# Optimization experiments

Measured on AMD Instinct MI355X. Metric: run time of the kernel, lower is better.

Reference implementation:

```python
import jax, jax.numpy as jnp
import numpy as np

# dims
B, S, V, H, D, I, L, SL, P = 1, 2048, 32000, 1024, 512, 4096, 2, 32, 4096
DECAY_FAST, DECAY_SLOW, CONS_RATE, CONS_EVERY = 0.9, 0.99, 0.1, 10


def _ln(x, g, b):
    m = x.mean(-1, keepdims=True)
    v = ((x - m) ** 2).mean(-1, keepdims=True)
    return (x - m) * jax.lax.rsqrt(v + 1e-5) * g + b


def _memory_scan(items, gates, fast0, slow0):
    # items [B,S,D], gates [B,S,SL]; sequential per-timestep memory update
    cons = (jnp.arange(items.shape[1]) % CONS_EVERY) == 0
    def step(carry, x):
        fast, slow = carry
        item, gate, c = x
        fast = DECAY_FAST * fast + gate[:, :, None] * item[:, None, :]
        slow = jnp.where(c, DECAY_SLOW * slow + CONS_RATE * fast, slow)
        fast = jnp.where(c, (1.0 - CONS_RATE) * fast, fast)
        return (fast, slow), None
    (fast, slow), _ = jax.lax.scan(
        step, (fast0, slow0),
        (items.transpose(1, 0, 2), gates.transpose(1, 0, 2), cons))
    return fast, slow


def _forward(input_ids, fast_states, slow_states, emb, pos_emb, W_item, b_item,
             W_q, b_q, rh_W1, rh_b1, rh_W2, rh_b2, gate_W, gate_b, W_out, b_out,
             ln1_g, ln1_b, ffn_W1, ffn_b1, ffn_W2, ffn_b2, ln2_g, ln2_b, fln_g, fln_b):
    b, s = input_ids.shape
    h = emb[input_ids] + pos_emb[:s][None]  # [B,S,H]
    new_fast, new_slow = [], []
    for l in range(W_item.shape[0]):
        items = h @ W_item[l] + b_item[l]          # [B,S,D]
        query = h @ W_q[l] + b_q[l]                # [B,S,H]
        # retrieval head -> unit-norm unbinding keys
        k1 = jax.nn.gelu(items @ rh_W1[l] + rh_b1[l])
        keys = k1 @ rh_W2[l] + rh_b2[l]
        keys = keys / (jnp.linalg.norm(keys, axis=-1, keepdims=True) + 1e-6)
        fast0, slow0 = fast_states[l], slow_states[l]  # [B,SL,D]
        # retrieval uses the initial (constant-within-sequence) states, so it
        # vectorizes over seq: slot attention + hadamard unbinding
        mem = jnp.concatenate([fast0, slow0], axis=1)  # [B,2*SL,D]
        scores = jnp.einsum('bsd,bnd->bsn', keys, mem) / jnp.sqrt(jnp.float32(D))
        attn = jax.nn.softmax(scores, axis=-1)
        retrieved = jnp.einsum('bsn,bnd->bsd', attn, mem) * keys  # [B,S,D]
        gates = jax.nn.sigmoid(jnp.concatenate([h, retrieved], -1) @ gate_W[l] + gate_b[l])
        fast_gates = gates[..., :SL]
        fast, slow = _memory_scan(items, fast_gates, fast0, slow0)
        new_fast.append(fast)
        new_slow.append(slow)
        out = jnp.concatenate([query, retrieved], -1) @ W_out[l] + b_out[l]
        h = _ln(h + out, ln1_g[l], ln1_b[l])
        ffn = jax.nn.gelu(h @ ffn_W1[l] + ffn_b1[l]) @ ffn_W2[l] + ffn_b2[l]
        h = _ln(h + ffn, ln2_g[l], ln2_b[l])
    h = _ln(h, fln_g, fln_b)
    logits = jnp.einsum('bsh,vh->bsv', h, emb)  # tied lm_head
    return logits, jnp.stack(new_fast), jnp.stack(new_slow)


def setup_inputs() -> dict:
    key = jax.random.key(0)
    def rn(i, shape, scale=0.02):
        return jax.random.normal(jax.random.fold_in(key, i), shape, dtype=jnp.float32) * scale
    z = lambda shape: jnp.zeros(shape, jnp.float32)
    return dict(
        input_ids=jax.random.randint(jax.random.fold_in(key, 0), (B, S), 0, V),
        fast_states=rn(100, (L, B, SL, D), 0.5),
        slow_states=rn(101, (L, B, SL, D), 0.5),
        emb=rn(1, (V, H)),
        pos_emb=rn(2, (P, H)),
        W_item=rn(3, (L, H, D)), b_item=z((L, D)),
        W_q=rn(4, (L, H, H)), b_q=z((L, H)),
        rh_W1=rn(5, (L, D, 2 * D)), rh_b1=z((L, 2 * D)),
        rh_W2=rn(6, (L, 2 * D, D)), rh_b2=z((L, D)),
        gate_W=rn(7, (L, H + D, 2 * SL)), gate_b=z((L, 2 * SL)),
        W_out=rn(8, (L, H + D, H)), b_out=z((L, H)),
        ln1_g=jnp.ones((L, H)), ln1_b=z((L, H)),
        ffn_W1=rn(9, (L, H, I)), ffn_b1=z((L, I)),
        ffn_W2=rn(10, (L, I, H)), ffn_b2=z((L, H)),
        ln2_g=jnp.ones((L, H)), ln2_b=z((L, H)),
        fln_g=jnp.ones((H,)), fln_b=z((H,)),
    )


def reference(input_ids, fast_states, slow_states, emb, pos_emb, W_item, b_item,
              W_q, b_q, rh_W1, rh_b1, rh_W2, rh_b2, gate_W, gate_b, W_out, b_out,
              ln1_g, ln1_b, ffn_W1, ffn_b1, ffn_W2, ffn_b2, ln2_g, ln2_b, fln_g, fln_b):
    return _forward(input_ids, fast_states, slow_states, emb, pos_emb, W_item, b_item,
                    W_q, b_q, rh_W1, rh_b1, rh_W2, rh_b2, gate_W, gate_b, W_out, b_out,
                    ln1_g, ln1_b, ffn_W1, ffn_b1, ffn_W2, ffn_b2, ln2_g, ln2_b, fln_g, fln_b)
```

## Files before the change

kernel.cpp:

```cpp
#include <hip/hip_runtime.h>
#include <hip/hip_bf16.h>
#include <stdint.h>

typedef __hip_bfloat16 bf16;
typedef float f32x4 __attribute__((ext_vector_type(4)));
typedef short s16x8 __attribute__((ext_vector_type(8)));
typedef short s16x4 __attribute__((ext_vector_type(4)));

#define DEV __device__ __forceinline__

static constexpr int S_ = 2048, H_ = 1024, D_ = 512, I_ = 4096, V_ = 32000;
static constexpr int SLn = 32, Lc = 2;
static constexpr size_t LOGITS_N = (size_t)S_ * V_;

DEV float gelu_f(float x) {
    float x3 = x * x * x;
    return 0.5f * x * (1.f + tanhf(0.7978845608028654f * (x + 0.044715f * x3)));
}

#define AS1(p) ((const __attribute__((address_space(1))) void*)(uintptr_t)(p))
#define AS3(p) ((__attribute__((address_space(3))) void*)(uint32_t)(uintptr_t)(p))

template <int BM, int BN, int TH, int WM, int WN, int FLAGS>
__global__ __launch_bounds__(TH, (TH == 512) ? 2 : 3) void gemm_p4(
    const bf16* __restrict__ A, int lda, const bf16* __restrict__ BT,
    const float* __restrict__ bias, float* __restrict__ Cf, int ldf,
    bf16* __restrict__ Cb, int ldb2, int K, int Mt, int Nt) {
    constexpr int FM = BM / (WM * 16), FN = BN / (WN * 16);
    constexpr int CA = (BM * 4) / TH, CB = (BN * 4) / TH, CH = CA + CB;
    constexpr int BUFS = (BM + BN) * 32;
    __shared__ short lds[4 * BUFS];
    const int tid = threadIdx.x, lane = tid & 63;
    const int wm = (tid >> 6) / WN, wn = (tid >> 6) % WN;

    int nwg = Mt * Nt;
    int bid = blockIdx.x, wgid = bid;
    if ((nwg & 7) == 0) {
        int cpx = nwg >> 3;
        wgid = (bid & 7) * cpx + (bid >> 3);
    }
    const int m0 = (wgid % Mt) * BM, n0 = (wgid / Mt) * BN;

    const bf16* aS[CA];
    const bf16* bS[CB];
#pragma unroll
    for (int c = 0; c < CA; ++c) {
        int L = (c * TH + tid) * 16;
        int sidx = L >> 10, w = L & 1023;
        int r16 = w >> 6;
        int c2 = (w & 63) ^ (((r16 >> 3) & 1) << 5);
        aS[c] = A + (size_t)(m0 + sidx * 16 + r16) * lda + (c2 >> 1);
    }
#pragma unroll
    for (int c = 0; c < CB; ++c) {
        int L = (c * TH + tid) * 16;
        int sidx = L >> 10, w = L & 1023;
        int r16 = w >> 6;
        int c2 = (w & 63) ^ (((r16 >> 3) & 1) << 5);
        bS[c] = BT + (size_t)(n0 + sidx * 16 + r16) * K + (c2 >> 1);
    }

    auto stage = [&](int kt) {
        short* dst = &lds[(kt & 3) * BUFS];
#pragma unroll
        for (int c = 0; c < CA; ++c)
            __builtin_amdgcn_global_load_lds(AS1(aS[c] + kt * 32), AS3(dst + (c * TH + tid) * 8), 16, 0, 0);
        short* dstB = dst + BM * 32;
#pragma unroll
        for (int c = 0; c < CB; ++c)
            __builtin_amdgcn_global_load_lds(AS1(bS[c] + kt * 32), AS3(dstB + (c * TH + tid) * 8), 16, 0, 0);
    };

    const int laneoff = ((lane & 15) * 64 + ((((lane >> 4) * 8) ^ (((lane >> 3) & 1) << 4)) << 1)) >> 1;

    f32x4 acc[FM][FN];
#pragma unroll
    for (int i = 0; i < FM; i++)
#pragma unroll
        for (int j = 0; j < FN; j++)
#pragma unroll
            for (int r = 0; r < 4; r++) acc[i][j][r] = 0.f;

    const int NT = K >> 5;
    stage(0);
    stage(1);
    stage(2);
    for (int t = 0; t < NT; ++t) {
        if (t + 3 < NT) stage(t + 3);
        const int rem = NT - 1 - t;
        if (rem >= 3)
            asm volatile("s_waitcnt vmcnt(%0)" ::"n"(3 * CH) : "memory");
        else if (rem == 2)
            asm volatile("s_waitcnt vmcnt(%0)" ::"n"(2 * CH) : "memory");
        else if (rem == 1)
            asm volatile("s_waitcnt vmcnt(%0)" ::"n"(CH) : "memory");
        else
            asm volatile("s_waitcnt vmcnt(0)" ::: "memory");
        __builtin_amdgcn_s_barrier();

        const short* as = &lds[(t & 3) * BUFS];
        const short* bs = as + BM * 32;
        s16x8 af[FM], bf[FN];
#pragma unroll
        for (int i = 0; i < FM; i++) af[i] = *(const s16x8*)&as[(wm * FM + i) * 512 + laneoff];
#pragma unroll
        for (int j = 0; j < FN; j++) bf[j] = *(const s16x8*)&bs[(wn * FN + j) * 512 + laneoff];
        __builtin_amdgcn_s_setprio(1);
#pragma unroll
        for (int i = 0; i < FM; i++)
#pragma unroll
            for (int j = 0; j < FN; j++)
                acc[i][j] = __builtin_amdgcn_mfma_f32_16x16x32_bf16(af[i], bf[j], acc[i][j], 0, 0, 0);
        __builtin_amdgcn_s_setprio(0);
        __builtin_amdgcn_s_barrier();
    }

#pragma unroll
    for (int i = 0; i < FM; i++) {
        int gr0 = m0 + (wm * FM + i) * 16 + ((lane >> 4) << 2);
#pragma unroll
        for (int j = 0; j < FN; j++) {
            int gc = n0 + (wn * FN + j) * 16 + (lane & 15);
            float bv = (FLAGS & 1) ? bias[gc] : 0.f;
#pragma unroll
            for (int r = 0; r < 4; r++) {
                float v = acc[i][j][r] + bv;
                if (FLAGS & 2) v = gelu_f(v);
                if (FLAGS & 4) Cf[(size_t)(gr0 + r) * ldf + gc] = v;
                if (FLAGS & 8) Cb[(size_t)(gr0 + r) * ldb2 + gc] = __float2bfloat16(v);
            }
        }
    }
}

__global__ __launch_bounds__(256) void transpose_bf16_kernel(const float* __restrict__ W,
                                                             bf16* __restrict__ WT, int K, int N) {
    __shared__ float t[32][33];
    int tx = threadIdx.x & 31, ty = threadIdx.x >> 5;
    int kb = blockIdx.y * 32, nb = blockIdx.x * 32;
#pragma unroll
    for (int i = 0; i < 4; i++)
        t[ty + 8 * i][tx] = W[(size_t)(kb + ty + 8 * i) * N + nb + tx];
    __syncthreads();
#pragma unroll
    for (int i = 0; i < 4; i++)
        WT[(size_t)(nb + ty + 8 * i) * K + kb + tx] = __float2bfloat16(t[tx][ty + 8 * i]);
}

__global__ void conv_bf16_kernel(const float* __restrict__ src, bf16* __restrict__ dst) {
    size_t i = (size_t)blockIdx.x * 256 + threadIdx.x;
    f32x4 v = ((const f32x4*)src)[i];
    s16x4 o;
#pragma unroll
    for (int j = 0; j < 4; j++) {
        bf16 h = __float2bfloat16(v[j]);
        o[j] = *(short*)&h;
    }
    ((s16x4*)dst)[i] = o;
}

__global__ void embed_kernel(const int* __restrict__ ids, const float* __restrict__ emb,
                             const float* __restrict__ pos, float* __restrict__ hF,
                             bf16* __restrict__ hB) {
    int t = blockIdx.x, tid = threadIdx.x;
    int id = ids[t];
    f32x4 v = ((const f32x4*)(emb + (size_t)id * H_))[tid];
    f32x4 q = ((const f32x4*)(pos + (size_t)t * H_))[tid];
    v = v + q;
    ((f32x4*)(hF + (size_t)t * H_))[tid] = v;
    s16x4 o;
#pragma unroll
    for (int j = 0; j < 4; j++) {
        bf16 h = __float2bfloat16(v[j]);
        o[j] = *(short*)&h;
    }
    ((s16x4*)(hB + (size_t)t * 1536))[tid] = o;
}

__global__ __launch_bounds__(256) void ln_kernel(const float* __restrict__ x,
                                                 const float* __restrict__ res,
                                                 const float* __restrict__ g,
                                                 const float* __restrict__ b,
                                                 float* __restrict__ of, bf16* __restrict__ ob,
                                                 int ldo) {
    __shared__ float red[8];
    int row = blockIdx.x, tid = threadIdx.x, lane = tid & 63, wid = tid >> 6;
    const float* xr = x + (size_t)row * H_;
    float v[4];
#pragma unroll
    for (int j = 0; j < 4; j++) {
        int c = tid + 256 * j;
        v[j] = xr[c] + (res ? res[(size_t)row * H_ + c] : 0.f);
    }
    float s = v[0] + v[1] + v[2] + v[3];
#pragma unroll
    for (int o = 32; o; o >>= 1) s += __shfl_xor(s, o);
    if (!lane) red[wid] = s;
    __syncthreads();
    float mean = (red[0] + red[1] + red[2] + red[3]) * (1.f / H_);
    float q = 0.f;
#pragma unroll
    for (int j = 0; j < 4; j++) {
        float d = v[j] - mean;
        q += d * d;
    }
#pragma unroll
    for (int o = 32; o; o >>= 1) q += __shfl_xor(q, o);
    if (!lane) red[4 + wid] = q;
    __syncthreads();
    float var = (red[4] + red[5] + red[6] + red[7]) * (1.f / H_);
    float rstd = rsqrtf(var + 1e-5f);
#pragma unroll
    for (int j = 0; j < 4; j++) {
        int c = tid + 256 * j;
        float o2 = (v[j] - mean) * rstd * g[c] + b[c];
        if (of) of[(size_t)row * H_ + c] = o2;
        if (ob) ob[(size_t)row * ldo + c] = __float2bfloat16(o2);
    }
}

__global__ void memt_kernel(const float* __restrict__ fast0, const float* __restrict__ slow0,
                            float* __restrict__ memT) {
    int idx = blockIdx.x * 256 + threadIdx.x;
    int d = idx >> 6, n = idx & 63;
    const float* m = (n < 32) ? fast0 + (size_t)n * D_ : slow0 + (size_t)(n - 32) * D_;
    memT[idx] = m[d];
}

__global__ __launch_bounds__(256) void attn_kernel(const float* __restrict__ keys,
                                                   const float* __restrict__ memT,
                                                   const float* __restrict__ fast0,
                                                   const float* __restrict__ slow0,
                                                   bf16* __restrict__ qr, bf16* __restrict__ hr) {
    __shared__ float klds[4][512];
    int wid = threadIdx.x >> 6, lane = threadIdx.x & 63;
    int r = blockIdx.x * 4 + wid;
    float kv[8], ss = 0.f;
#pragma unroll
    for (int j = 0; j < 8; j++) {
        kv[j] = keys[(size_t)r * D_ + lane + 64 * j];
        ss += kv[j] * kv[j];
    }
#pragma unroll
    for (int o = 32; o; o >>= 1) ss += __shfl_xor(ss, o);
    float inv = 1.f / (sqrtf(ss) + 1e-6f);
#pragma unroll
    for (int j = 0; j < 8; j++) {
        kv[j] *= inv;
        klds[wid][lane + 64 * j] = kv[j];
    }
    __syncthreads();
    float s0 = 0.f, s1 = 0.f, s2 = 0.f, s3 = 0.f;
#pragma unroll 8
    for (int d = 0; d < 512; d += 4) {
        s0 = fmaf(klds[wid][d + 0], memT[(d + 0) * 64 + lane], s0);
        s1 = fmaf(klds[wid][d + 1], memT[(d + 1) * 64 + lane], s1);
        s2 = fmaf(klds[wid][d + 2], memT[(d + 2) * 64 + lane], s2);
        s3 = fmaf(klds[wid][d + 3], memT[(d + 3) * 64 + lane], s3);
    }
    float s = (s0 + s1 + s2 + s3) * 0.044194173824159216f;
    float m = s;
#pragma unroll
    for (int o = 32; o; o >>= 1) m = fmaxf(m, __shfl_xor(m, o));
    float p = expf(s - m);
    float sum = p;
#pragma unroll
    for (int o = 32; o; o >>= 1) sum += __shfl_xor(sum, o);
    float pn = p / sum;
    float rv[8];
#pragma unroll
    for (int j = 0; j < 8; j++) rv[j] = 0.f;
    for (int n2 = 0; n2 < 64; ++n2) {
        float a2 = __shfl(pn, n2);
        const float* m2 = (n2 < 32) ? (fast0 + (size_t)n2 * D_) : (slow0 + (size_t)(n2 - 32) * D_);
#pragma unroll
        for (int j = 0; j < 8; j++) rv[j] = fmaf(a2, m2[lane + 64 * j], rv[j]);
    }
#pragma unroll
    for (int j = 0; j < 8; j++) {
        bf16 o = __float2bfloat16(rv[j] * kv[j]);
        qr[(size_t)r * 1536 + 1024 + lane + 64 * j] = o;
        hr[(size_t)r * 1536 + 1024 + lane + 64 * j] = o;
    }
}

__global__ void coef_kernel(float* __restrict__ coef) {
    int t = blockIdx.x * 256 + threadIdx.x;
    int j0 = (t + 9) / 10;
    float a = powf(0.9f, (float)(2047 - t + 205 - j0));
    float b = 0.f;
    for (int j = j0; j < 205; ++j)
        b += powf(0.9f, (float)(10 * j - t + j - j0)) * powf(0.99f, (float)(204 - j));
    b *= 0.1f;
    coef[t] = a;
    coef[2048 + t] = b;
    if (t == 0) {
        coef[4096] = powf(0.99f, 205.f);
        float cfs = 0.f;
        for (int j = 0; j < 205; ++j)
            cfs += powf(0.9f, (float)(11 * j + 1)) * powf(0.99f, (float)(204 - j));
        coef[4097] = 0.1f * cfs;
    }
}

__global__ void sigcoef_kernel(const float* __restrict__ raw, const float* __restrict__ coef,
                               float* __restrict__ ga, float* __restrict__ gb) {
    int i = blockIdx.x * 256 + threadIdx.x;
    int r = i >> 5, n = i & 31;
    float g = 1.f / (1.f + expf(-raw[r * 64 + n]));
    ga[i] = g * coef[r];
    gb[i] = g * coef[2048 + r];
}

__global__ __launch_bounds__(256) void scan_part_kernel(const float* __restrict__ items,
                                                        const float* __restrict__ ga,
                                                        const float* __restrict__ gb,
                                                        float* __restrict__ pF,
                                                        float* __restrict__ pS) {
    int tid = threadIdx.x;
    int d = (blockIdx.x & 7) * 64 + (tid & 63);
    int mg = (blockIdx.x >> 3) & 1;
    int tc = blockIdx.x >> 4;
    int m0 = mg * 16 + (tid >> 6) * 4;
    float aF[4] = {0.f, 0.f, 0.f, 0.f}, aS[4] = {0.f, 0.f, 0.f, 0.f};
    for (int t = tc * 128; t < tc * 128 + 128; ++t) {
        float it = items[(size_t)t * D_ + d];
#pragma unroll
        for (int j = 0; j < 4; j++) {
            aF[j] = fmaf(ga[t * 32 + m0 + j], it, aF[j]);
            aS[j] = fmaf(gb[t * 32 + m0 + j], it, aS[j]);
        }
    }
#pragma unroll
    for (int j = 0; j < 4; j++) {
        pF[((size_t)tc * 32 + m0 + j) * D_ + d] = aF[j];
        pS[((size_t)tc * 32 + m0 + j) * D_ + d] = aS[j];
    }
}

__global__ __launch_bounds__(256) void scan_reduce_kernel(const float* __restrict__ pF,
                                                          const float* __restrict__ pS,
                                                          const float* __restrict__ coef,
                                                          const float* __restrict__ fast0,
                                                          const float* __restrict__ slow0,
                                                          float* __restrict__ fastO,
                                                          float* __restrict__ slowO) {
    int i = blockIdx.x * 256 + threadIdx.x;
    float f = 0.f, s = 0.f;
#pragma unroll
    for (int c = 0; c < 16; c++) {
        f += pF[(size_t)c * 32 * D_ + i];
        s += pS[(size_t)c * 32 * D_ + i];
    }
    fastO[i] = f;
    slowO[i] = s + coef[4096] * slow0[i] + coef[4097] * fast0[i];
}

static inline void gemmM(hipStream_t st, const bf16* A, int lda, const bf16* BT,
                         const float* bias, float* Cf, int ldf, bf16* Cb, int ldb2,
                         int M, int N, int K, int flags) {
    int Mt = M / 128, Nt = N / 64;
    dim3 g(Mt * Nt), b(256);
#define GCASE(fl)                                                                             \
    if (flags == fl) {                                                                        \
        gemm_p4<128, 64, 256, 2, 2, fl><<<g, b, 0, st>>>(A, lda, BT, bias, Cf, ldf, Cb, ldb2, \
                                                         K, Mt, Nt);                          \
        return;                                                                               \
    }
    GCASE(13)
    GCASE(9)
    GCASE(11)
    GCASE(5)
#undef GCASE
}

static inline void transp(hipStream_t st, const float* W, bf16* WT, int K, int N) {
    transpose_bf16_kernel<<<dim3(N / 32, K / 32), 256, 0, st>>>(W, WT, K, N);
}

extern "C" void kernel_launch(void* const* d_in, const int* in_sizes, int n_in,
                              void* d_out, int out_size, void* d_ws, size_t ws_size,
                              hipStream_t stream) {
    const int* ids = (const int*)d_in[0];
    const float* fastS = (const float*)d_in[1];
    const float* slowS = (const float*)d_in[2];
    const float* emb = (const float*)d_in[3];
    const float* pos = (const float*)d_in[4];
    const float* W_item = (const float*)d_in[5];
    const float* b_item = (const float*)d_in[6];
    const float* W_q = (const float*)d_in[7];
    const float* b_q = (const float*)d_in[8];
    const float* rh_W1 = (const float*)d_in[9];
    const float* rh_b1 = (const float*)d_in[10];
    const float* rh_W2 = (const float*)d_in[11];
    const float* rh_b2 = (const float*)d_in[12];
    const float* gate_W = (const float*)d_in[13];
    const float* gate_b = (const float*)d_in[14];
    const float* W_out = (const float*)d_in[15];
    const float* b_out = (const float*)d_in[16];
    const float* ln1_g = (const float*)d_in[17];
    const float* ln1_b = (const float*)d_in[18];
    const float* ffn_W1 = (const float*)d_in[19];
    const float* ffn_b1 = (const float*)d_in[20];
    const float* ffn_W2 = (const float*)d_in[21];
    const float* ffn_b2 = (const float*)d_in[22];
    const float* ln2_g = (const float*)d_in[23];
    const float* ln2_b = (const float*)d_in[24];
    const float* fln_g = (const float*)d_in[25];
    const float* fln_b = (const float*)d_in[26];
    float* outP = (float*)d_out;

    size_t off = 0;
    char* base = (char*)d_ws;
    auto alloc = [&](size_t n) -> char* {
        char* p = base + off;
        off += (n + 255) & ~(size_t)255;
        return p;
    };
    bf16* wItemT = (bf16*)alloc((size_t)Lc * D_ * H_ * 2);
    bf16* wQT = (bf16*)alloc((size_t)Lc * H_ * H_ * 2);
    bf16* rh1T = (bf16*)alloc((size_t)Lc * (2 * D_) * D_ * 2);
    bf16* rh2T = (bf16*)alloc((size_t)Lc * D_ * (2 * D_) * 2);
    bf16* wOutT = (bf16*)alloc((size_t)Lc * H_ * 1536 * 2);
    bf16* f1T = (bf16*)alloc((size_t)Lc * I_ * H_ * 2);
    bf16* f2T = (bf16*)alloc((size_t)Lc * H_ * I_ * 2);
    bf16* gWT = (bf16*)alloc((size_t)Lc * 64 * 1536 * 2);
    bf16* embB = (bf16*)alloc((size_t)V_ * H_ * 2);
    float* hF = (float*)alloc((size_t)S_ * H_ * 4);
    bf16* hrB = (bf16*)alloc((size_t)S_ * 1536 * 2);
    bf16* hB = hrB;
    float* itemsF = (float*)alloc((size_t)S_ * D_ * 4);
    bf16* itemsB = (bf16*)alloc((size_t)S_ * D_ * 2);
    bf16* qrB = (bf16*)alloc((size_t)S_ * 1536 * 2);
    bf16* k1B = (bf16*)alloc((size_t)S_ * (2 * D_) * 2);
    float* keysF = (float*)alloc((size_t)S_ * D_ * 4);
    float* outF = (float*)alloc((size_t)S_ * H_ * 4);
    bf16* ffn1B = (bf16*)alloc((size_t)S_ * I_ * 2);
    float* gRawF = (float*)alloc((size_t)S_ * 64 * 4);
    float* gaF = (float*)alloc((size_t)S_ * SLn * 4);
    float* gbF = (float*)alloc((size_t)S_ * SLn * 4);
    float* coefF = (float*)alloc(4200 * 4);
    float* memT = (float*)alloc((size_t)D_ * 64 * 4);
    float* pF = (float*)alloc((size_t)16 * SLn * D_ * 4);
    float* pS = (float*)alloc((size_t)16 * SLn * D_ * 4);

    coef_kernel<<<8, 256, 0, stream>>>(coefF);
    for (int l = 0; l < Lc; ++l) {
        transp(stream, W_item + (size_t)l * H_ * D_, wItemT + (size_t)l * D_ * H_, H_, D_);
        transp(stream, W_q + (size_t)l * H_ * H_, wQT + (size_t)l * H_ * H_, H_, H_);
        transp(stream, rh_W1 + (size_t)l * D_ * 2 * D_, rh1T + (size_t)l * 2 * D_ * D_, D_, 2 * D_);
        transp(stream, rh_W2 + (size_t)l * 2 * D_ * D_, rh2T + (size_t)l * D_ * 2 * D_, 2 * D_, D_);
        transp(stream, W_out + (size_t)l * 1536 * H_, wOutT + (size_t)l * H_ * 1536, 1536, H_);
        transp(stream, ffn_W1 + (size_t)l * H_ * I_, f1T + (size_t)l * I_ * H_, H_, I_);
        transp(stream, ffn_W2 + (size_t)l * I_ * H_, f2T + (size_t)l * H_ * I_, I_, H_);
        transp(stream, gate_W + (size_t)l * 1536 * 64, gWT + (size_t)l * 64 * 1536, 1536, 64);
    }
    conv_bf16_kernel<<<(int)((size_t)V_ * H_ / 4 / 256), 256, 0, stream>>>(emb, embB);
    embed_kernel<<<S_, 256, 0, stream>>>(ids, emb, pos, hF, hB);

    for (int l = 0; l < Lc; ++l) {
        const float* fast0 = fastS + (size_t)l * SLn * D_;
        const float* slow0 = slowS + (size_t)l * SLn * D_;
        gemmM(stream, hB, 1536, wItemT + (size_t)l * D_ * H_, b_item + l * D_, itemsF, D_,
              itemsB, D_, S_, D_, H_, 13);
        gemmM(stream, hB, 1536, wQT + (size_t)l * H_ * H_, b_q + l * H_, nullptr, 0, qrB, 1536,
              S_, H_, H_, 9);
        gemmM(stream, itemsB, D_, rh1T + (size_t)l * 2 * D_ * D_, rh_b1 + l * 2 * D_, nullptr, 0,
              k1B, 2 * D_, S_, 2 * D_, D_, 11);
        gemmM(stream, k1B, 2 * D_, rh2T + (size_t)l * D_ * 2 * D_, rh_b2 + l * D_, keysF, D_,
              nullptr, 0, S_, D_, 2 * D_, 5);
        memt_kernel<<<128, 256, 0, stream>>>(fast0, slow0, memT);
        attn_kernel<<<S_ / 4, 256, 0, stream>>>(keysF, memT, fast0, slow0, qrB, hrB);
        gemmM(stream, hrB, 1536, gWT + (size_t)l * 64 * 1536, gate_b + l * 64, gRawF, 64,
              nullptr, 0, S_, 64, 1536, 5);
        sigcoef_kernel<<<S_ * SLn / 256, 256, 0, stream>>>(gRawF, coefF, gaF, gbF);
        scan_part_kernel<<<256, 256, 0, stream>>>(itemsF, gaF, gbF, pF, pS);
        scan_reduce_kernel<<<64, 256, 0, stream>>>(
            pF, pS, coefF, fast0, slow0, outP + LOGITS_N + (size_t)l * SLn * D_,
            outP + LOGITS_N + (size_t)Lc * SLn * D_ + (size_t)l * SLn * D_);
        gemmM(stream, qrB, 1536, wOutT + (size_t)l * H_ * 1536, b_out + l * H_, outF, H_,
              nullptr, 0, S_, H_, 1536, 5);
        ln_kernel<<<S_, 256, 0, stream>>>(hF, outF, ln1_g + l * H_, ln1_b + l * H_, hF, hB, 1536);
        gemmM(stream, hB, 1536, f1T + (size_t)l * I_ * H_, ffn_b1 + l * I_, nullptr, 0, ffn1B,
              I_, S_, I_, H_, 11);
        gemmM(stream, ffn1B, I_, f2T + (size_t)l * H_ * I_, ffn_b2 + l * H_, outF, H_, nullptr,
              0, S_, H_, I_, 5);
        ln_kernel<<<S_, 256, 0, stream>>>(hF, outF, ln2_g + l * H_, ln2_b + l * H_, hF, hB, 1536);
    }
    ln_kernel<<<S_, 256, 0, stream>>>(hF, nullptr, fln_g, fln_b, nullptr, hB, 1536);
    gemm_p4<256, 256, 512, 2, 4, 4><<<1000, 512, 0, stream>>>(hB, 1536, embB, nullptr, outP, V_,
                                                              nullptr, 0, H_, 8, 125);
}
```

Measured before the change: 937.5 us.

## Split GEMM k-step into two phases interleaving A/B prefetch with MFMA

The GEMM main loop is restructured so the wait for the next k-tile happens at the end of the current iteration rather than the start. For large tiles (the 256x256 logits GEMM) the MFMA work is split into two phases, with the A and B prefetches issued separately between them. This aims to overlap global-to-LDS loads with matrix math and cut barrier stalls. It adds extra barriers per iteration and tighter vmcnt accounting, with a risk of races if the counts are wrong.

```diff
diff --git a/kernel.cpp b/kernel.cpp
--- a/kernel.cpp
+++ b/kernel.cpp
@@ -22,12 +22,14 @@
 #define AS3(p) ((__attribute__((address_space(3))) void*)(uint32_t)(uintptr_t)(p))
 
 template <int BM, int BN, int TH, int WM, int WN, int FLAGS>
-__global__ __launch_bounds__(TH, (TH == 512) ? 2 : 3) void gemm_p4(
+__global__ __launch_bounds__(TH, (TH == 512) ? 2 : 3) void gemm_p5(
     const bf16* __restrict__ A, int lda, const bf16* __restrict__ BT,
     const float* __restrict__ bias, float* __restrict__ Cf, int ldf,
     bf16* __restrict__ Cb, int ldb2, int K, int Mt, int Nt) {
     constexpr int FM = BM / (WM * 16), FN = BN / (WN * 16);
     constexpr int CA = (BM * 4) / TH, CB = (BN * 4) / TH, CH = CA + CB;
+    constexpr int NPH = (FM * FN >= 32) ? 2 : 1;
+    constexpr int FMP = FM / NPH;
     constexpr int BUFS = (BM + BN) * 32;
     __shared__ short lds[4 * BUFS];
     const int tid = threadIdx.x, lane = tid & 63;
@@ -60,15 +62,17 @@
         bS[c] = BT + (size_t)(n0 + sidx * 16 + r16) * K + (c2 >> 1);
     }
 
-    auto stage = [&](int kt) {
+    auto stageA = [&](int kt) {
         short* dst = &lds[(kt & 3) * BUFS];
 #pragma unroll
         for (int c = 0; c < CA; ++c)
             __builtin_amdgcn_global_load_lds(AS1(aS[c] + kt * 32), AS3(dst + (c * TH + tid) * 8), 16, 0, 0);
-        short* dstB = dst + BM * 32;
+    };
+    auto stageB = [&](int kt) {
+        short* dst = &lds[(kt & 3) * BUFS + BM * 32];
 #pragma unroll
         for (int c = 0; c < CB; ++c)
-            __builtin_amdgcn_global_load_lds(AS1(bS[c] + kt * 32), AS3(dstB + (c * TH + tid) * 8), 16, 0, 0);
+            __builtin_amdgcn_global_load_lds(AS1(bS[c] + kt * 32), AS3(dst + (c * TH + tid) * 8), 16, 0, 0);
     };
 
     const int laneoff = ((lane & 15) * 64 + ((((lane >> 4) * 8) ^ (((lane >> 3) & 1) << 4)) << 1)) >> 1;
@@ -82,37 +86,58 @@
             for (int r = 0; r < 4; r++) acc[i][j][r] = 0.f;
 
     const int NT = K >> 5;
-    stage(0);
-    stage(1);
-    stage(2);
+    stageA(0); stageB(0);
+    stageA(1); stageB(1);
+    stageA(2); stageB(2);
+    asm volatile("s_waitcnt vmcnt(%0)" ::"n"(2 * CH) : "memory");
+    __builtin_amdgcn_s_barrier();
+
     for (int t = 0; t < NT; ++t) {
-        if (t + 3 < NT) stage(t + 3);
-        const int rem = NT - 1 - t;
-        if (rem >= 3)
-            asm volatile("s_waitcnt vmcnt(%0)" ::"n"(3 * CH) : "memory");
-        else if (rem == 2)
-            asm volatile("s_waitcnt vmcnt(%0)" ::"n"(2 * CH) : "memory");
-        else if (rem == 1)
-            asm volatile("s_waitcnt vmcnt(%0)" ::"n"(CH) : "memory");
-        else
-            asm volatile("s_waitcnt vmcnt(0)" ::: "memory");
-        __builtin_amdgcn_s_barrier();
-
         const short* as = &lds[(t & 3) * BUFS];
         const short* bs = as + BM * 32;
-        s16x8 af[FM], bf[FN];
-#pragma unroll
-        for (int i = 0; i < FM; i++) af[i] = *(const s16x8*)&as[(wm * FM + i) * 512 + laneoff];
-#pragma unroll
-        for (int j = 0; j < FN; j++) bf[j] = *(const s16x8*)&bs[(wn * FN + j) * 512 + laneoff];
-        __builtin_amdgcn_s_setprio(1);
-#pragma unroll
-        for (int i = 0; i < FM; i++)
-#pragma unroll
-            for (int j = 0; j < FN; j++)
-                acc[i][j] = __builtin_amdgcn_mfma_f32_16x16x32_bf16(af[i], bf[j], acc[i][j], 0, 0, 0);
-        __builtin_amdgcn_s_setprio(0);
-        __builtin_amdgcn_s_barrier();
+        s16x8 bf[FN];
+#pragma unroll
+        for (int p = 0; p < NPH; ++p) {
+            s16x8 af[FMP];
+#pragma unroll
+            for (int i = 0; i < FMP; i++)
+                af[i] = *(const s16x8*)&as[(wm * FM + p * FMP + i) * 512 + laneoff];
+            if (p == 0) {
+#pragma unroll
+                for (int j = 0; j < FN; j++)
+                    bf[j] = *(const s16x8*)&bs[(wn * FN + j) * 512 + laneoff];
+            }
+            if (t + 3 < NT) {
+                if (NPH == 1) {
+                    stageA(t + 3);
+                    stageB(t + 3);
+                } else if (p == 0) {
+                    stageA(t + 3);
+                } else {
+                    stageB(t + 3);
+                }
+            }
+            if (p == NPH - 1 && t + 1 < NT) {
+                const int ahead = NT - 2 - t;
+                if (ahead >= 2)
+                    asm volatile("s_waitcnt vmcnt(%0)" ::"n"(2 * CH) : "memory");
+                else if (ahead == 1)
+                    asm volatile("s_waitcnt vmcnt(%0)" ::"n"(CH) : "memory");
+                else
+                    asm volatile("s_waitcnt vmcnt(0)" ::: "memory");
+            }
+            __builtin_amdgcn_s_barrier();
+            __builtin_amdgcn_sched_barrier(0);
+            __builtin_amdgcn_s_setprio(1);
+#pragma unroll
+            for (int i = 0; i < FMP; i++)
+#pragma unroll
+                for (int j = 0; j < FN; j++)
+                    acc[p * FMP + i][j] =
+                        __builtin_amdgcn_mfma_f32_16x16x32_bf16(af[i], bf[j], acc[p * FMP + i][j], 0, 0, 0);
+            __builtin_amdgcn_s_setprio(0);
+            __builtin_amdgcn_s_barrier();
+        }
     }
 
 #pragma unroll
@@ -363,7 +388,7 @@
     dim3 g(Mt * Nt), b(256);
 #define GCASE(fl)                                                                             \
     if (flags == fl) {                                                                        \
-        gemm_p4<128, 64, 256, 2, 2, fl><<<g, b, 0, st>>>(A, lda, BT, bias, Cf, ldf, Cb, ldb2, \
+        gemm_p5<128, 64, 256, 2, 2, fl><<<g, b, 0, st>>>(A, lda, BT, bias, Cf, ldf, Cb, ldb2, \
                                                          K, Mt, Nt);                          \
         return;                                                                               \
     }
@@ -488,6 +513,6 @@
         ln_kernel<<<S_, 256, 0, stream>>>(hF, outF, ln2_g + l * H_, ln2_b + l * H_, hF, hB, 1536);
     }
     ln_kernel<<<S_, 256, 0, stream>>>(hF, nullptr, fln_g, fln_b, nullptr, hB, 1536);
-    gemm_p4<256, 256, 512, 2, 4, 4><<<1000, 512, 0, stream>>>(hB, 1536, embB, nullptr, outP, V_,
+    gemm_p5<256, 256, 512, 2, 4, 4><<<1000, 512, 0, stream>>>(hB, 1536, embB, nullptr, outP, V_,
                                                               nullptr, 0, H_, 8, 125);
 }
```

Result: no change. 923.8 us (-1.5%).
